# Kernel optimization log

Hardware: AMD Instinct MI355X
Metric: run time of the kernel (lower is better)

## Reference

```python
import jax, jax.numpy as jnp
import numpy as np

E = 1024
H = 16
CH = E // H

def setup_inputs() -> dict:
    key = jax.random.key(0)
    ks = jax.random.split(key, 9)
    s = E ** -0.5
    return {
        'x': jax.random.normal(ks[0], (4, 2048, E), dtype=jnp.float32),
        'Wq': jax.random.normal(ks[1], (E, E), dtype=jnp.float32) * s,
        'bq': jnp.zeros((E,), dtype=jnp.float32),
        'Wk': jax.random.normal(ks[2], (E, E), dtype=jnp.float32) * s,
        'bk': jnp.zeros((E,), dtype=jnp.float32),
        'Wv': jax.random.normal(ks[3], (E, E), dtype=jnp.float32) * s,
        'bv': jnp.zeros((E,), dtype=jnp.float32),
        'Wo': jax.random.normal(ks[4], (E, E), dtype=jnp.float32) * s,
        'bo': jnp.zeros((E,), dtype=jnp.float32),
    }

def _split_heads(t):
    # [..., n, H*ch] -> [..., H, n, ch]
    b, n, e = t.shape
    return t.reshape(b, n, H, CH).transpose(0, 2, 1, 3)

def reference(x, Wq, bq, Wk, bk, Wv, bv, Wo, bo):
    scale = CH ** -0.5
    q = _split_heads(x @ Wq.T + bq)  # [b,H,n,ch]
    k = _split_heads(x @ Wk.T + bk)
    v = _split_heads(x @ Wv.T + bv)
    att = jnp.einsum('bhqc,bhkc->bhqk', q, k) * scale
    att = jax.nn.softmax(att, axis=-1)
    out = jnp.einsum('bhqk,bhkc->bhqc', att, v)  # [b,H,n,ch]
    b, h, n, c = out.shape
    out = out.transpose(0, 2, 1, 3).reshape(b, n, h * c)
    return out @ Wo.T + bo
```

## Files before the change

kernel.cpp:

```cpp
#include <hip/hip_runtime.h>
#include <stdint.h>

#define EMB   1024
#define NHEAD 16
#define CHD   64
#define NB    4
#define SEQ   2048
#define NTOK  (NB * SEQ)
#define KDIM  1024

typedef __attribute__((ext_vector_type(8)))  short bf16x8;
typedef __attribute__((ext_vector_type(4)))  short short4v;
typedef __attribute__((ext_vector_type(4)))  float f32x4;
typedef __attribute__((ext_vector_type(16))) float f32x16;
typedef __attribute__((ext_vector_type(4)))  float float4v;

__device__ __forceinline__ short f2bf(float f) {
    unsigned int u = __float_as_uint(f);
    u += 0x7fffu + ((u >> 16) & 1u);
    return (short)(u >> 16);
}

__device__ __forceinline__ void async16(const short* g, short* l) {
    __builtin_amdgcn_global_load_lds((__attribute__((address_space(1))) void const*)g,
                                     (__attribute__((address_space(3))) void*)l, 16, 0, 0);
}

__global__ __launch_bounds__(256) void cvt_all(const float* __restrict__ x,
                                               const float* __restrict__ Wq,
                                               const float* __restrict__ Wk,
                                               const float* __restrict__ Wv,
                                               const float* __restrict__ Wo,
                                               short* __restrict__ xb,
                                               short* __restrict__ Wqb,
                                               short* __restrict__ Wkb,
                                               short* __restrict__ Wvb,
                                               short* __restrict__ Wob) {
    int bid = blockIdx.x;
    const float* src;
    short* dst;
    int idx;
    if (bid < 8192) {
        src = x; dst = xb; idx = bid * 256 + threadIdx.x;
    } else {
        int w  = (bid - 8192) >> 10;
        int lb = (bid - 8192) & 1023;
        src = (w == 0) ? Wq : (w == 1) ? Wk : (w == 2) ? Wv : Wo;
        dst = (w == 0) ? Wqb : (w == 1) ? Wkb : (w == 2) ? Wvb : Wob;
        idx = lb * 256 + threadIdx.x;
    }
    float4v v = ((const float4v*)src)[idx];
    short4v s;
    s.x = f2bf(v.x); s.y = f2bf(v.y); s.z = f2bf(v.z); s.w = f2bf(v.w);
    ((short4v*)dst)[idx] = s;
}

__device__ __forceinline__ void gemm_core(const short* __restrict__ Atile,
                                          const short* __restrict__ Btile,
                                          short* As, short* Bs, f32x4 acc[4][4]) {
    const int tid  = threadIdx.x;
    const int wave = tid >> 6, lane = tid & 63;
    const int quad = lane >> 4, l16 = lane & 15;
    const int wm = (wave >> 1) * 64, wn = (wave & 1) * 64;
    const int srow = lane >> 2;
    const int scol = (lane & 3) * 8;

    for (int k0 = 0; k0 < KDIM; k0 += 32) {
        __syncthreads();
#pragma unroll
        for (int c = 0; c < 2; ++c) {
            int chunk = wave * 2 + c;
            int row = chunk * 16 + srow;
            async16(Atile + (size_t)row * KDIM + k0 + scol, As + chunk * 512);
            async16(Btile + (size_t)row * KDIM + k0 + scol, Bs + chunk * 512);
        }
        __syncthreads();
        bf16x8 af[4], bfr[4];
#pragma unroll
        for (int i = 0; i < 4; ++i)
            af[i] = *(const bf16x8*)&As[(wm + i * 16 + l16) * 32 + quad * 8];
#pragma unroll
        for (int j = 0; j < 4; ++j)
            bfr[j] = *(const bf16x8*)&Bs[(wn + j * 16 + l16) * 32 + quad * 8];
#pragma unroll
        for (int i = 0; i < 4; ++i)
#pragma unroll
            for (int j = 0; j < 4; ++j)
                acc[i][j] = __builtin_amdgcn_mfma_f32_16x16x32_bf16(af[i], bfr[j], acc[i][j], 0, 0, 0);
    }
}

#define QSCALE 0.1803368801111204f
__global__ __launch_bounds__(256) void qkv_gemm(const short* __restrict__ xb,
                                                const short* __restrict__ Wqb,
                                                const short* __restrict__ Wkb,
                                                const short* __restrict__ Wvb,
                                                const float* __restrict__ bq,
                                                const float* __restrict__ bk,
                                                const float* __restrict__ bv,
                                                short* __restrict__ Qb,
                                                short* __restrict__ Kb,
                                                short* __restrict__ Vtb) {
    __shared__ short As[128 * 32], Bs[128 * 32];
    const int bm = blockIdx.x, bn = blockIdx.y;
    const int which = bn >> 3;
    const int ew = (bn & 7) * 128;
    const short* W    = (which == 0) ? Wqb : (which == 1) ? Wkb : Wvb;
    const float* bias = (which == 0) ? bq  : (which == 1) ? bk  : bv;
    const float sc    = (which == 0) ? QSCALE : 1.0f;

    const short* Xt = xb + (size_t)bm * 128 * KDIM;
    const short* Wt = W + (size_t)ew * KDIM;
    const short* Ap = (which == 2) ? Wt : Xt;
    const short* Bp = (which == 2) ? Xt : Wt;

    f32x4 acc[4][4];
    const f32x4 z = {0.f, 0.f, 0.f, 0.f};
#pragma unroll
    for (int i = 0; i < 4; ++i)
#pragma unroll
        for (int j = 0; j < 4; ++j) acc[i][j] = z;

    gemm_core(Ap, Bp, As, Bs, acc);

    const int lane = threadIdx.x & 63, wave = threadIdx.x >> 6;
    const int quad = lane >> 4, l16 = lane & 15;
    const int wm = (wave >> 1) * 64, wn = (wave & 1) * 64;

    if (which == 2) {
#pragma unroll
        for (int i = 0; i < 4; ++i)
#pragma unroll
            for (int j = 0; j < 4; ++j)
#pragma unroll
                for (int r = 0; r < 4; ++r) {
                    int e = ew + wm + i * 16 + quad * 4 + r;
                    int token = bm * 128 + wn + j * 16 + l16;
                    int bb = token >> 11, nn = token & 2047;
                    int hh = e >> 6, cc = e & 63;
                    Vtb[(((size_t)bb * NHEAD + hh) * CHD + cc) * SEQ + nn] =
                        f2bf(acc[i][j][r] + bias[e]);
                }
    } else {
        short* dst = which ? Kb : Qb;
#pragma unroll
        for (int i = 0; i < 4; ++i)
#pragma unroll
            for (int j = 0; j < 4; ++j)
#pragma unroll
                for (int r = 0; r < 4; ++r) {
                    int token = bm * 128 + wm + i * 16 + quad * 4 + r;
                    int bb = token >> 11, nn = token & 2047;
                    int e = ew + wn + j * 16 + l16;
                    int hh = e >> 6, cc = e & 63;
                    dst[(((size_t)bb * NHEAD + hh) * SEQ + nn) * CHD + cc] =
                        f2bf((acc[i][j][r] + bias[e]) * sc);
                }
    }
}

__global__ __launch_bounds__(128, 1) void attn(const short* __restrict__ Qb,
                                               const short* __restrict__ Kb,
                                               const short* __restrict__ Vtb,
                                               short* __restrict__ AOb) {
    __shared__ short Ks[16 * 512];
    __shared__ short Vs[16 * 512];

    const int qt = blockIdx.x;
    const int bh = blockIdx.y;
    const int tid = threadIdx.x, wave = tid >> 6, lane = tid & 63;
    const int l31 = lane & 31, h = lane >> 5;

    const short* Kg = Kb  + (size_t)bh * SEQ * CHD;
    const short* Vg = Vtb + (size_t)bh * CHD * SEQ;

    bf16x8 qf[2][4];
#pragma unroll
    for (int g = 0; g < 2; ++g)
#pragma unroll
        for (int c = 0; c < 4; ++c)
            qf[g][c] = *(const bf16x8*)(Qb + ((size_t)bh * SEQ + qt * 128 + wave * 64 + g * 32 + l31) * CHD
                                        + c * 16 + h * 8);

    int koff[8], voff[8];
#pragma unroll
    for (int cc = 0; cc < 8; ++cc) {
        int c = wave * 8 + cc;
        int l = c * 8 + (lane >> 3);
        int w = l & 31, r = w & 3, hh = (w >> 2) & 1, t = w >> 3, T = l >> 5;
        int gkv = 32 * T + 16 * (t >> 1) + 8 * hh + 4 * (t & 1) + 2 * (r >> 1) + (r & 1);
        koff[cc] = gkv * CHD + (((lane & 7) ^ (l & 7)) << 3);
        int ch = c * 4 + (lane >> 4);
        voff[cc] = ch * SEQ + (((lane & 15) ^ (ch & 15)) << 3);
    }

    int kra[4];
#pragma unroll
    for (int c = 0; c < 4; ++c)
        kra[c] = l31 * 64 + ((((2 * c + h) ^ (l31 & 7))) << 3);
    int vra[2];
#pragma unroll
    for (int s = 0; s < 2; ++s)
        vra[s] = l31 * 128 + ((((2 * s + h) ^ (l31 & 15))) << 3);

    const f32x16 z16 = {0.f,0.f,0.f,0.f,0.f,0.f,0.f,0.f,0.f,0.f,0.f,0.f,0.f,0.f,0.f,0.f};
    f32x16 O[2][2];
    O[0][0] = z16; O[0][1] = z16; O[1][0] = z16; O[1][1] = z16;
    float ls[2] = {0.f, 0.f};

    const short* Kgp = Kg;
    const short* Vgp = Vg;

    for (int kt = 0; kt < 16; ++kt) {
        __syncthreads();
#pragma unroll
        for (int cc = 0; cc < 8; ++cc) {
            int c = wave * 8 + cc;
            async16(Kgp + koff[cc], Ks + c * 512);
            async16(Vgp + voff[cc], Vs + c * 512);
        }
        Kgp += 128 * CHD;
        Vgp += 128;
        __syncthreads();

#pragma unroll
        for (int T = 0; T < 4; ++T) {
            f32x16 s0, s1;
            {
                bf16x8 kf = *(const bf16x8*)(Ks + kra[0] + T * 2048);
                s0 = __builtin_amdgcn_mfma_f32_32x32x16_bf16(kf, qf[0][0], z16, 0, 0, 0);
                s1 = __builtin_amdgcn_mfma_f32_32x32x16_bf16(kf, qf[1][0], z16, 0, 0, 0);
            }
#pragma unroll
            for (int c = 1; c < 4; ++c) {
                bf16x8 kf = *(const bf16x8*)(Ks + kra[c] + T * 2048);
                s0 = __builtin_amdgcn_mfma_f32_32x32x16_bf16(kf, qf[0][c], s0, 0, 0, 0);
                s1 = __builtin_amdgcn_mfma_f32_32x32x16_bf16(kf, qf[1][c], s1, 0, 0, 0);
            }

            bf16x8 pf[2][2];
#pragma unroll
            for (int g = 0; g < 2; ++g) {
                const f32x16 sg = g ? s1 : s0;
                float lacc = 0.f;
#pragma unroll
                for (int sg2 = 0; sg2 < 2; ++sg2) {
                    unsigned u[8];
#pragma unroll
                    for (int e = 0; e < 8; ++e)
                        u[e] = __float_as_uint(__builtin_amdgcn_exp2f(sg[sg2 * 8 + e]));
                    union { int i[4]; bf16x8 v; } pk;
                    pk.i[0] = __builtin_amdgcn_perm(u[1], u[0], 0x07060302u);
                    pk.i[1] = __builtin_amdgcn_perm(u[3], u[2], 0x07060302u);
                    pk.i[2] = __builtin_amdgcn_perm(u[5], u[4], 0x07060302u);
                    pk.i[3] = __builtin_amdgcn_perm(u[7], u[6], 0x07060302u);
                    pf[g][sg2] = pk.v;
                    float a0 = __uint_as_float(u[0] & 0xffff0000u) + __uint_as_float(u[1] & 0xffff0000u);
                    float a1 = __uint_as_float(u[2] & 0xffff0000u) + __uint_as_float(u[3] & 0xffff0000u);
                    float a2 = __uint_as_float(u[4] & 0xffff0000u) + __uint_as_float(u[5] & 0xffff0000u);
                    float a3 = __uint_as_float(u[6] & 0xffff0000u) + __uint_as_float(u[7] & 0xffff0000u);
                    lacc += (a0 + a1) + (a2 + a3);
                }
                ls[g] += lacc;
            }

#pragma unroll
            for (int sg2 = 0; sg2 < 2; ++sg2) {
                int vo = (vra[sg2] ^ (T << 5));
#pragma unroll
                for (int ct = 0; ct < 2; ++ct) {
                    bf16x8 vf = *(const bf16x8*)(Vs + vo + ct * 4096);
                    O[0][ct] = __builtin_amdgcn_mfma_f32_32x32x16_bf16(pf[0][sg2], vf, O[0][ct], 0, 0, 0);
                    O[1][ct] = __builtin_amdgcn_mfma_f32_32x32x16_bf16(pf[1][sg2], vf, O[1][ct], 0, 0, 0);
                }
            }
        }
    }

    float lt[2];
#pragma unroll
    for (int g = 0; g < 2; ++g) {
        lt[g] = ls[g] + __shfl_xor(ls[g], 32);
        lt[g] = 1.0f / lt[g];
    }

    const int b = bh >> 4, hd = bh & 15;
#pragma unroll
    for (int g = 0; g < 2; ++g)
#pragma unroll
        for (int reg = 0; reg < 16; ++reg) {
            int qr = (reg & 3) + 8 * (reg >> 2) + 4 * h;
            float li = __shfl(lt[g], qr);
            int n = qt * 128 + wave * 64 + g * 32 + qr;
#pragma unroll
            for (int ct = 0; ct < 2; ++ct) {
                int ccol = ct * 32 + l31;
                AOb[((size_t)b * SEQ + n) * EMB + hd * CHD + ccol] = f2bf(O[g][ct][reg] * li);
            }
        }
}

__global__ __launch_bounds__(256) void out_gemm(const short* __restrict__ AOb,
                                                const short* __restrict__ Wob,
                                                const float* __restrict__ bo,
                                                float* __restrict__ out) {
    __shared__ short As[128 * 32], Bs[128 * 32];
    const int bm = blockIdx.x, bn = blockIdx.y;

    f32x4 acc[4][4];
    const f32x4 z = {0.f, 0.f, 0.f, 0.f};
#pragma unroll
    for (int i = 0; i < 4; ++i)
#pragma unroll
        for (int j = 0; j < 4; ++j) acc[i][j] = z;

    gemm_core(AOb + (size_t)bm * 128 * KDIM, Wob + (size_t)bn * 128 * KDIM, As, Bs, acc);

    const int lane = threadIdx.x & 63, wave = threadIdx.x >> 6;
    const int quad = lane >> 4, l16 = lane & 15;
    const int wm = (wave >> 1) * 64, wn = (wave & 1) * 64;
#pragma unroll
    for (int i = 0; i < 4; ++i)
#pragma unroll
        for (int j = 0; j < 4; ++j)
#pragma unroll
            for (int r = 0; r < 4; ++r) {
                int token = bm * 128 + wm + i * 16 + quad * 4 + r;
                int e = bn * 128 + wn + j * 16 + l16;
                out[(size_t)token * EMB + e] = acc[i][j][r] + bo[e];
            }
}

extern "C" void kernel_launch(void* const* d_in, const int* in_sizes, int n_in,
                              void* d_out, int out_size, void* d_ws, size_t ws_size,
                              hipStream_t stream) {
    const float* x  = (const float*)d_in[0];
    const float* Wq = (const float*)d_in[1];
    const float* bq = (const float*)d_in[2];
    const float* Wk = (const float*)d_in[3];
    const float* bk = (const float*)d_in[4];
    const float* Wv = (const float*)d_in[5];
    const float* bv = (const float*)d_in[6];
    const float* Wo = (const float*)d_in[7];
    const float* bo = (const float*)d_in[8];

    char* ws = (char*)d_ws;
    short* xb  = (short*)(ws + 0);
    short* Wqb = (short*)(ws + (size_t)16 * 1024 * 1024);
    short* Wkb = (short*)(ws + (size_t)18 * 1024 * 1024);
    short* Wvb = (short*)(ws + (size_t)20 * 1024 * 1024);
    short* Wob = (short*)(ws + (size_t)22 * 1024 * 1024);
    short* Qb  = (short*)(ws + (size_t)24 * 1024 * 1024);
    short* Kb  = (short*)(ws + (size_t)40 * 1024 * 1024);
    short* Vtb = (short*)(ws + (size_t)56 * 1024 * 1024);
    short* AOb = (short*)(ws + (size_t)72 * 1024 * 1024);

    cvt_all<<<dim3(8192 + 4096), dim3(256), 0, stream>>>(x, Wq, Wk, Wv, Wo,
                                                         xb, Wqb, Wkb, Wvb, Wob);
    qkv_gemm<<<dim3(64, 24), dim3(256), 0, stream>>>(xb, Wqb, Wkb, Wvb, bq, bk, bv, Qb, Kb, Vtb);
    attn<<<dim3(16, 64), dim3(128), 0, stream>>>(Qb, Kb, Vtb, AOb);
    out_gemm<<<dim3(64, 8), dim3(256), 0, stream>>>(AOb, Wob, bo, (float*)d_out);
}
```

Measured before the change: 315.0 us.

## Double-buffer K/V tiles in attention and deepen GEMM K-step to 64

The attention kernel now double-buffers its K and V shared-memory tiles. The next tile's async global-to-LDS loads are issued before computing on the current tile, and one barrier per iteration is dropped, so global latency can overlap with MFMA work. The shared GEMM core now stages 64-wide K slices instead of 32, which halves the number of barrier pairs and doubles the MFMAs per sync. In exchange, LDS use doubles in both kernels, the new 128-byte row stride may cause more bank conflicts, and the overlap depends on the compiler not inserting a full vmcnt wait before the LDS reads.

```diff
diff --git a/kernel.cpp b/kernel.cpp
--- a/kernel.cpp
+++ b/kernel.cpp
@@ -62,31 +62,37 @@
     const int wave = tid >> 6, lane = tid & 63;
     const int quad = lane >> 4, l16 = lane & 15;
     const int wm = (wave >> 1) * 64, wn = (wave & 1) * 64;
-    const int srow = lane >> 2;
-    const int scol = (lane & 3) * 8;
-
-    for (int k0 = 0; k0 < KDIM; k0 += 32) {
+    const int srow = lane >> 3;
+    const int scol = (lane & 7) * 8;
+
+    for (int k0 = 0; k0 < KDIM; k0 += 64) {
         __syncthreads();
 #pragma unroll
-        for (int c = 0; c < 2; ++c) {
-            int chunk = wave * 2 + c;
-            int row = chunk * 16 + srow;
+        for (int c = 0; c < 4; ++c) {
+            int chunk = wave * 4 + c;
+            int row = chunk * 8 + srow;
             async16(Atile + (size_t)row * KDIM + k0 + scol, As + chunk * 512);
             async16(Btile + (size_t)row * KDIM + k0 + scol, Bs + chunk * 512);
         }
         __syncthreads();
-        bf16x8 af[4], bfr[4];
-#pragma unroll
-        for (int i = 0; i < 4; ++i)
-            af[i] = *(const bf16x8*)&As[(wm + i * 16 + l16) * 32 + quad * 8];
-#pragma unroll
-        for (int j = 0; j < 4; ++j)
-            bfr[j] = *(const bf16x8*)&Bs[(wn + j * 16 + l16) * 32 + quad * 8];
-#pragma unroll
-        for (int i = 0; i < 4; ++i)
-#pragma unroll
-            for (int j = 0; j < 4; ++j)
-                acc[i][j] = __builtin_amdgcn_mfma_f32_16x16x32_bf16(af[i], bfr[j], acc[i][j], 0, 0, 0);
+        bf16x8 af[4][2], bfr[4][2];
+#pragma unroll
+        for (int i = 0; i < 4; ++i) {
+            af[i][0] = *(const bf16x8*)&As[(wm + i * 16 + l16) * 64 + quad * 8];
+            af[i][1] = *(const bf16x8*)&As[(wm + i * 16 + l16) * 64 + 32 + quad * 8];
+        }
+#pragma unroll
+        for (int j = 0; j < 4; ++j) {
+            bfr[j][0] = *(const bf16x8*)&Bs[(wn + j * 16 + l16) * 64 + quad * 8];
+            bfr[j][1] = *(const bf16x8*)&Bs[(wn + j * 16 + l16) * 64 + 32 + quad * 8];
+        }
+#pragma unroll
+        for (int c = 0; c < 2; ++c)
+#pragma unroll
+            for (int i = 0; i < 4; ++i)
+#pragma unroll
+                for (int j = 0; j < 4; ++j)
+                    acc[i][j] = __builtin_amdgcn_mfma_f32_16x16x32_bf16(af[i][c], bfr[j][c], acc[i][j], 0, 0, 0);
     }
 }
 
@@ -101,7 +107,7 @@
                                                 short* __restrict__ Qb,
                                                 short* __restrict__ Kb,
                                                 short* __restrict__ Vtb) {
-    __shared__ short As[128 * 32], Bs[128 * 32];
+    __shared__ short As[128 * 64], Bs[128 * 64];
     const int bm = blockIdx.x, bn = blockIdx.y;
     const int which = bn >> 3;
     const int ew = (bn & 7) * 128;
@@ -163,8 +169,8 @@
                                                const short* __restrict__ Kb,
                                                const short* __restrict__ Vtb,
                                                short* __restrict__ AOb) {
-    __shared__ short Ks[16 * 512];
-    __shared__ short Vs[16 * 512];
+    __shared__ short Ks[2 * 16 * 512];
+    __shared__ short Vs[2 * 16 * 512];
 
     const int qt = blockIdx.x;
     const int bh = blockIdx.y;
@@ -208,32 +214,43 @@
     O[0][0] = z16; O[0][1] = z16; O[1][0] = z16; O[1][1] = z16;
     float ls[2] = {0.f, 0.f};
 
-    const short* Kgp = Kg;
-    const short* Vgp = Vg;
+#pragma unroll
+    for (int cc = 0; cc < 8; ++cc) {
+        int c = wave * 8 + cc;
+        async16(Kg + koff[cc], Ks + c * 512);
+        async16(Vg + voff[cc], Vs + c * 512);
+    }
+    const short* Kgp = Kg + 128 * CHD;
+    const short* Vgp = Vg + 128;
 
     for (int kt = 0; kt < 16; ++kt) {
         __syncthreads();
-#pragma unroll
-        for (int cc = 0; cc < 8; ++cc) {
-            int c = wave * 8 + cc;
-            async16(Kgp + koff[cc], Ks + c * 512);
-            async16(Vgp + voff[cc], Vs + c * 512);
-        }
-        Kgp += 128 * CHD;
-        Vgp += 128;
-        __syncthreads();
+        short* Kcur = Ks + (kt & 1) * 8192;
+        short* Vcur = Vs + (kt & 1) * 8192;
+        if (kt < 15) {
+            short* Knx = Ks + ((kt + 1) & 1) * 8192;
+            short* Vnx = Vs + ((kt + 1) & 1) * 8192;
+#pragma unroll
+            for (int cc = 0; cc < 8; ++cc) {
+                int c = wave * 8 + cc;
+                async16(Kgp + koff[cc], Knx + c * 512);
+                async16(Vgp + voff[cc], Vnx + c * 512);
+            }
+            Kgp += 128 * CHD;
+            Vgp += 128;
+        }
 
 #pragma unroll
         for (int T = 0; T < 4; ++T) {
             f32x16 s0, s1;
             {
-                bf16x8 kf = *(const bf16x8*)(Ks + kra[0] + T * 2048);
+                bf16x8 kf = *(const bf16x8*)(Kcur + kra[0] + T * 2048);
                 s0 = __builtin_amdgcn_mfma_f32_32x32x16_bf16(kf, qf[0][0], z16, 0, 0, 0);
                 s1 = __builtin_amdgcn_mfma_f32_32x32x16_bf16(kf, qf[1][0], z16, 0, 0, 0);
             }
 #pragma unroll
             for (int c = 1; c < 4; ++c) {
-                bf16x8 kf = *(const bf16x8*)(Ks + kra[c] + T * 2048);
+                bf16x8 kf = *(const bf16x8*)(Kcur + kra[c] + T * 2048);
                 s0 = __builtin_amdgcn_mfma_f32_32x32x16_bf16(kf, qf[0][c], s0, 0, 0, 0);
                 s1 = __builtin_amdgcn_mfma_f32_32x32x16_bf16(kf, qf[1][c], s1, 0, 0, 0);
             }
@@ -269,7 +286,7 @@
                 int vo = (vra[sg2] ^ (T << 5));
 #pragma unroll
                 for (int ct = 0; ct < 2; ++ct) {
-                    bf16x8 vf = *(const bf16x8*)(Vs + vo + ct * 4096);
+                    bf16x8 vf = *(const bf16x8*)(Vcur + vo + ct * 4096);
                     O[0][ct] = __builtin_amdgcn_mfma_f32_32x32x16_bf16(pf[0][sg2], vf, O[0][ct], 0, 0, 0);
                     O[1][ct] = __builtin_amdgcn_mfma_f32_32x32x16_bf16(pf[1][sg2], vf, O[1][ct], 0, 0, 0);
                 }
@@ -304,7 +321,7 @@
                                                 const short* __restrict__ Wob,
                                                 const float* __restrict__ bo,
                                                 float* __restrict__ out) {
-    __shared__ short As[128 * 32], Bs[128 * 32];
+    __shared__ short As[128 * 64], Bs[128 * 64];
     const int bm = blockIdx.x, bn = blockIdx.y;
 
     f32x4 acc[4][4];
```

New measurement: 328.8 us. 4.4% more time.

## Double-buffer K/V tiles and widen attention blocks to four waves

Applied to the files above, without the earlier changes.

The attention kernel now runs 256-thread blocks that cover 256 queries, so each K/V tile staged in shared memory is reused by four waves instead of two. The K/V shared buffers are doubled so the next tile's async global-to-LDS loads are issued while the current tile is being computed. This removes one barrier per iteration and the load stall before the matmuls. In exchange it uses 64KB of LDS per block and halves the grid, which may limit occupancy and load balance across CUs.

```diff
diff --git a/kernel.cpp b/kernel.cpp
--- a/kernel.cpp
+++ b/kernel.cpp
@@ -159,12 +159,12 @@
     }
 }
 
-__global__ __launch_bounds__(128, 1) void attn(const short* __restrict__ Qb,
+__global__ __launch_bounds__(256, 2) void attn(const short* __restrict__ Qb,
                                                const short* __restrict__ Kb,
                                                const short* __restrict__ Vtb,
                                                short* __restrict__ AOb) {
-    __shared__ short Ks[16 * 512];
-    __shared__ short Vs[16 * 512];
+    __shared__ short Ks[2 * 16 * 512];
+    __shared__ short Vs[2 * 16 * 512];
 
     const int qt = blockIdx.x;
     const int bh = blockIdx.y;
@@ -179,13 +179,13 @@
     for (int g = 0; g < 2; ++g)
 #pragma unroll
         for (int c = 0; c < 4; ++c)
-            qf[g][c] = *(const bf16x8*)(Qb + ((size_t)bh * SEQ + qt * 128 + wave * 64 + g * 32 + l31) * CHD
+            qf[g][c] = *(const bf16x8*)(Qb + ((size_t)bh * SEQ + qt * 256 + wave * 64 + g * 32 + l31) * CHD
                                         + c * 16 + h * 8);
 
-    int koff[8], voff[8];
-#pragma unroll
-    for (int cc = 0; cc < 8; ++cc) {
-        int c = wave * 8 + cc;
+    int koff[4], voff[4];
+#pragma unroll
+    for (int cc = 0; cc < 4; ++cc) {
+        int c = wave * 4 + cc;
         int l = c * 8 + (lane >> 3);
         int w = l & 31, r = w & 3, hh = (w >> 2) & 1, t = w >> 3, T = l >> 5;
         int gkv = 32 * T + 16 * (t >> 1) + 8 * hh + 4 * (t & 1) + 2 * (r >> 1) + (r & 1);
@@ -208,32 +208,43 @@
     O[0][0] = z16; O[0][1] = z16; O[1][0] = z16; O[1][1] = z16;
     float ls[2] = {0.f, 0.f};
 
-    const short* Kgp = Kg;
-    const short* Vgp = Vg;
+#pragma unroll
+    for (int cc = 0; cc < 4; ++cc) {
+        int c = wave * 4 + cc;
+        async16(Kg + koff[cc], Ks + c * 512);
+        async16(Vg + voff[cc], Vs + c * 512);
+    }
+    const short* Kgp = Kg + 128 * CHD;
+    const short* Vgp = Vg + 128;
 
     for (int kt = 0; kt < 16; ++kt) {
         __syncthreads();
-#pragma unroll
-        for (int cc = 0; cc < 8; ++cc) {
-            int c = wave * 8 + cc;
-            async16(Kgp + koff[cc], Ks + c * 512);
-            async16(Vgp + voff[cc], Vs + c * 512);
+        const short* Kcur = Ks + (kt & 1) * 8192;
+        const short* Vcur = Vs + (kt & 1) * 8192;
+        if (kt < 15) {
+            short* Knx = Ks + ((kt + 1) & 1) * 8192;
+            short* Vnx = Vs + ((kt + 1) & 1) * 8192;
+#pragma unroll
+            for (int cc = 0; cc < 4; ++cc) {
+                int c = wave * 4 + cc;
+                async16(Kgp + koff[cc], Knx + c * 512);
+                async16(Vgp + voff[cc], Vnx + c * 512);
+            }
+            Kgp += 128 * CHD;
+            Vgp += 128;
         }
-        Kgp += 128 * CHD;
-        Vgp += 128;
-        __syncthreads();
 
 #pragma unroll
         for (int T = 0; T < 4; ++T) {
             f32x16 s0, s1;
             {
-                bf16x8 kf = *(const bf16x8*)(Ks + kra[0] + T * 2048);
+                bf16x8 kf = *(const bf16x8*)(Kcur + kra[0] + T * 2048);
                 s0 = __builtin_amdgcn_mfma_f32_32x32x16_bf16(kf, qf[0][0], z16, 0, 0, 0);
                 s1 = __builtin_amdgcn_mfma_f32_32x32x16_bf16(kf, qf[1][0], z16, 0, 0, 0);
             }
 #pragma unroll
             for (int c = 1; c < 4; ++c) {
-                bf16x8 kf = *(const bf16x8*)(Ks + kra[c] + T * 2048);
+                bf16x8 kf = *(const bf16x8*)(Kcur + kra[c] + T * 2048);
                 s0 = __builtin_amdgcn_mfma_f32_32x32x16_bf16(kf, qf[0][c], s0, 0, 0, 0);
                 s1 = __builtin_amdgcn_mfma_f32_32x32x16_bf16(kf, qf[1][c], s1, 0, 0, 0);
             }
@@ -269,7 +280,7 @@
                 int vo = (vra[sg2] ^ (T << 5));
 #pragma unroll
                 for (int ct = 0; ct < 2; ++ct) {
-                    bf16x8 vf = *(const bf16x8*)(Vs + vo + ct * 4096);
+                    bf16x8 vf = *(const bf16x8*)(Vcur + vo + ct * 4096);
                     O[0][ct] = __builtin_amdgcn_mfma_f32_32x32x16_bf16(pf[0][sg2], vf, O[0][ct], 0, 0, 0);
                     O[1][ct] = __builtin_amdgcn_mfma_f32_32x32x16_bf16(pf[1][sg2], vf, O[1][ct], 0, 0, 0);
                 }
@@ -291,7 +302,7 @@
         for (int reg = 0; reg < 16; ++reg) {
             int qr = (reg & 3) + 8 * (reg >> 2) + 4 * h;
             float li = __shfl(lt[g], qr);
-            int n = qt * 128 + wave * 64 + g * 32 + qr;
+            int n = qt * 256 + wave * 64 + g * 32 + qr;
 #pragma unroll
             for (int ct = 0; ct < 2; ++ct) {
                 int ccol = ct * 32 + l31;
@@ -358,6 +369,6 @@
     cvt_all<<<dim3(8192 + 4096), dim3(256), 0, stream>>>(x, Wq, Wk, Wv, Wo,
                                                          xb, Wqb, Wkb, Wvb, Wob);
     qkv_gemm<<<dim3(64, 24), dim3(256), 0, stream>>>(xb, Wqb, Wkb, Wvb, bq, bk, bv, Qb, Kb, Vtb);
-    attn<<<dim3(16, 64), dim3(128), 0, stream>>>(Qb, Kb, Vtb, AOb);
+    attn<<<dim3(8, 64), dim3(256), 0, stream>>>(Qb, Kb, Vtb, AOb);
     out_gemm<<<dim3(64, 8), dim3(256), 0, stream>>>(AOb, Wob, bo, (float*)d_out);
 }
```

Measured after the change: 325.6 us. 1.03x slower.
